# Optimization experiments

Hardware: AMD Instinct MI355X
Metric: run time of the kernel (lower is better)

The kernel has to match this reference:

```python
import jax, jax.numpy as jnp
import numpy as np

THRESHOLD = 0.3
STRENGTH = 0.1
MIN_S = 0.0
MAX_S = 0.5
EPS_COS = 1e-8
EPS_LN = 1e-5

B, T, D = 1024, 64, 256
P = 2048
H = 512


def _layernorm(x, g, b):
    mu = x.mean(-1, keepdims=True)
    var = ((x - mu) ** 2).mean(-1, keepdims=True)
    return (x - mu) * jax.lax.rsqrt(var + EPS_LN) * g + b


def setup_inputs() -> dict:
    key = jax.random.key(0)
    ks = jax.random.split(key, 10)
    s = lambda fan_in: 1.0 / np.sqrt(fan_in)
    return {
        "current_feat": jax.random.normal(ks[0], (B, T, D), jnp.float32),
        "prototype": jax.random.normal(ks[1], (P, T, D), jnp.float32),
        "dd_w1": jax.random.normal(ks[2], (2 * D, H), jnp.float32) * s(2 * D),
        "dd_b1": jnp.zeros((H,), jnp.float32),
        "dd_g1": jnp.ones((H,), jnp.float32),
        "dd_be1": jnp.zeros((H,), jnp.float32),
        "dd_w2": jax.random.normal(ks[3], (H, H // 2), jnp.float32) * s(H),
        "dd_b2": jnp.zeros((H // 2,), jnp.float32),
        "dd_w3": jax.random.normal(ks[4], (H // 2, 1), jnp.float32) * s(H // 2),
        "dd_b3": jnp.zeros((1,), jnp.float32),
        "cal_w1": jax.random.normal(ks[5], (D, H), jnp.float32) * s(D),
        "cal_b1": jnp.zeros((H,), jnp.float32),
        "cal_g1": jnp.ones((H,), jnp.float32),
        "cal_be1": jnp.zeros((H,), jnp.float32),
        "cal_w2": jax.random.normal(ks[6], (H, H), jnp.float32) * s(H),
        "cal_b2": jnp.zeros((H,), jnp.float32),
        "cal_w3": jax.random.normal(ks[7], (H, D), jnp.float32) * s(H),
        "cal_b3": jnp.zeros((D,), jnp.float32),
    }


def reference(current_feat, prototype,
              dd_w1, dd_b1, dd_g1, dd_be1, dd_w2, dd_b2, dd_w3, dd_b3,
              cal_w1, cal_b1, cal_g1, cal_be1, cal_w2, cal_b2, cal_w3, cal_b3):
    # --- drift detection ---
    feat_flat = current_feat.mean(axis=1)          # [B, D]
    proto_centers = prototype.mean(axis=1)         # [P, D]
    fn = jnp.maximum(jnp.linalg.norm(feat_flat, axis=-1), EPS_COS)   # [B]
    pn = jnp.maximum(jnp.linalg.norm(proto_centers, axis=-1), EPS_COS)  # [P]
    sim = jnp.einsum('bd,pd->bp', feat_flat, proto_centers) / (fn[:, None] * pn[None, :])
    drift_score = 1.0 - sim                        # [B, P]
    is_drifted = drift_score.mean(axis=0) > THRESHOLD  # [P] bool

    # --- calibration (batched over all P, then masked scatter) ---
    global_mean = feat_flat.mean(axis=0)           # [D]
    concat = jnp.concatenate(
        [proto_centers, jnp.broadcast_to(global_mean, (proto_centers.shape[0], global_mean.shape[0]))], axis=-1)  # [P, 2D]
    h = jax.nn.relu(_layernorm(concat @ dd_w1 + dd_b1, dd_g1, dd_be1))
    h = jax.nn.relu(h @ dd_w2 + dd_b2)
    drift_conf = jax.nn.sigmoid(h @ dd_w3 + dd_b3)[:, 0]  # [P]

    c = jax.nn.relu(_layernorm(proto_centers @ cal_w1 + cal_b1, cal_g1, cal_be1))
    c = jax.nn.relu(c @ cal_w2 + cal_b2)
    delta = c @ cal_w3 + cal_b3                    # [P, D]

    strength = jnp.clip(STRENGTH * drift_conf, MIN_S, MAX_S)  # [P]
    new_center = proto_centers + strength[:, None] * delta    # [P, D]

    calibrated = jnp.where(is_drifted[:, None, None], new_center[:, None, :], prototype)  # [P, T, D]
    return calibrated, drift_score, is_drifted
```

## Files before the change

kernel.cpp:

```cpp
#include <hip/hip_runtime.h>
#include <hip/hip_bf16.h>
#include <math.h>

#define BB 1024
#define TT 64
#define DD 256
#define PP 2048
#define HH 512

typedef __attribute__((ext_vector_type(8))) short short8;
typedef __attribute__((ext_vector_type(4))) float f32x4;

__device__ __forceinline__ float4 f4add(float4 a, float4 b) {
    return make_float4(a.x + b.x, a.y + b.y, a.z + b.z, a.w + b.w);
}

__device__ __forceinline__ void nt_store4(float* p, float4 v) {
    f32x4 t = {v.x, v.y, v.z, v.w};
    __builtin_nontemporal_store(t, (f32x4*)p);
}

__device__ __forceinline__ void nt_store1(float* p, float v) {
    __builtin_nontemporal_store(v, p);
}

__device__ __forceinline__ float blk_reduce(float v, float* sm) {
    int tid = threadIdx.x;
    #pragma unroll
    for (int o = 32; o > 0; o >>= 1) v += __shfl_down(v, o, 64);
    if ((tid & 63) == 0) sm[tid >> 6] = v;
    __syncthreads();
    float r = sm[0] + sm[1] + sm[2] + sm[3];
    __syncthreads();
    return r;
}

__device__ __forceinline__ float2 blk_reduce2(float a, float b, float* sm) {
    int tid = threadIdx.x;
    #pragma unroll
    for (int o = 32; o > 0; o >>= 1) {
        a += __shfl_down(a, o, 64);
        b += __shfl_down(b, o, 64);
    }
    if ((tid & 63) == 0) { sm[(tid >> 6) * 2] = a; sm[(tid >> 6) * 2 + 1] = b; }
    __syncthreads();
    float ra = sm[0] + sm[2] + sm[4] + sm[6];
    float rb = sm[1] + sm[3] + sm[5] + sm[7];
    __syncthreads();
    return make_float2(ra, rb);
}

__device__ __forceinline__ float row_mean_batch(const float* __restrict__ base,
                                                float* __restrict__ smr) {
    int tid = threadIdx.x;
    int c4 = tid & 63;
    int t0 = tid >> 6;
    const float* p = base + t0 * DD + (c4 << 2);
    float4 v[16];
    #pragma unroll
    for (int i = 0; i < 16; ++i)
        v[i] = *(const float4*)(p + (i << 2) * DD);
    #pragma unroll
    for (int i = 0; i < 8; ++i) v[i] = f4add(v[i], v[i + 8]);
    #pragma unroll
    for (int i = 0; i < 4; ++i) v[i] = f4add(v[i], v[i + 4]);
    float4 s = f4add(f4add(v[0], v[1]), f4add(v[2], v[3]));
    *(float4*)&smr[t0 * 256 + (c4 << 2)] = s;
    __syncthreads();
    return (smr[tid] + smr[256 + tid] + smr[512 + tid] + smr[768 + tid]) * (1.f / TT);
}

__global__ void prep_k(const float* __restrict__ cf, const float* __restrict__ proto,
                       const float* __restrict__ dd_w1, const float* __restrict__ dd_w2,
                       const float* __restrict__ cal_w1, const float* __restrict__ cal_w2,
                       const float* __restrict__ cal_w3,
                       float* __restrict__ ffm, float* __restrict__ fn,
                       float* __restrict__ pn, float* __restrict__ pc,
                       __hip_bfloat16* __restrict__ ffb, __hip_bfloat16* __restrict__ pcb,
                       __hip_bfloat16* __restrict__ w1cat, __hip_bfloat16* __restrict__ w2dd,
                       __hip_bfloat16* __restrict__ w2cal, __hip_bfloat16* __restrict__ w3cal) {
    __shared__ float smr[1024];
    __shared__ float sm[4];
    int b = blockIdx.x, tid = threadIdx.x;
    if (b < 1024) {
        float m = row_mean_batch(cf + (size_t)b * TT * DD, smr);
        ffm[(size_t)b * DD + tid] = m;
        ffb[(size_t)b * DD + tid] = __float2bfloat16(m);
        float q = m * m;
        #pragma unroll
        for (int o = 32; o > 0; o >>= 1) q += __shfl_down(q, o, 64);
        if ((tid & 63) == 0) sm[tid >> 6] = q;
        __syncthreads();
        if (tid == 0) fn[b] = fmaxf(sqrtf(sm[0] + sm[1] + sm[2] + sm[3]), 1e-8f);
    } else if (b < 3072) {
        int r = b - 1024;
        float m = row_mean_batch(proto + (size_t)r * TT * DD, smr);
        pc[(size_t)r * DD + tid] = m;
        pcb[(size_t)r * DD + tid] = __float2bfloat16(m);
        float q = m * m;
        #pragma unroll
        for (int o = 32; o > 0; o >>= 1) q += __shfl_down(q, o, 64);
        if ((tid & 63) == 0) sm[tid >> 6] = q;
        __syncthreads();
        if (tid == 0) pn[r] = fmaxf(sqrtf(sm[0] + sm[1] + sm[2] + sm[3]), 1e-8f);
    } else {
        int idx = (b - 3072) * 256 + tid;
        if (idx < 262144) {
            int half = idx >> 17;
            int i = idx & 131071;
            int n = i & 511, k = i >> 9;
            const float* src = half ? cal_w1 : dd_w1;
            w1cat[(size_t)(half * 512 + n) * 256 + k] = __float2bfloat16(src[(size_t)k * 512 + n]);
        } else if (idx < 393216) {
            int i = idx - 262144;
            int n = i & 255, k = i >> 8;
            w2dd[(size_t)n * 512 + k] = __float2bfloat16(dd_w2[(size_t)k * 256 + n]);
        } else if (idx < 655360) {
            int i = idx - 393216;
            int n = i & 511, k = i >> 9;
            w2cal[(size_t)n * 512 + k] = __float2bfloat16(cal_w2[(size_t)k * 512 + n]);
        } else {
            int i = idx - 655360;
            int n = i & 255, k = i >> 8;
            w3cal[(size_t)n * 512 + k] = __float2bfloat16(cal_w3[(size_t)k * 256 + n]);
        }
    }
}

__global__ void sim_addvec_k(const __hip_bfloat16* __restrict__ A,
                             const __hip_bfloat16* __restrict__ Bt,
                             const float* __restrict__ fn, const float* __restrict__ pn,
                             const float* __restrict__ ffm,
                             const float* __restrict__ dd_w1, const float* __restrict__ dd_b1,
                             float* __restrict__ drift, float* __restrict__ colsum,
                             float* __restrict__ addvec) {
    if (blockIdx.x >= 512) {
        __shared__ float gmk[256];
        int tid = threadIdx.x;
        const float* f = ffm + tid;
        float a0 = 0.f, a1 = 0.f, a2 = 0.f, a3 = 0.f, a4 = 0.f, a5 = 0.f, a6 = 0.f, a7 = 0.f;
        #pragma unroll 4
        for (int b = 0; b < 1024; b += 8) {
            a0 += f[(b + 0) << 8]; a1 += f[(b + 1) << 8];
            a2 += f[(b + 2) << 8]; a3 += f[(b + 3) << 8];
            a4 += f[(b + 4) << 8]; a5 += f[(b + 5) << 8];
            a6 += f[(b + 6) << 8]; a7 += f[(b + 7) << 8];
        }
        gmk[tid] = (((a0 + a1) + (a2 + a3)) + ((a4 + a5) + (a6 + a7))) * (1.f / BB);
        __syncthreads();
        int j = (blockIdx.x - 512) * 256 + tid;
        float s = dd_b1[j];
        #pragma unroll 8
        for (int k = 0; k < 256; ++k) s = fmaf(gmk[k], dd_w1[(size_t)(256 + k) * 512 + j], s);
        addvec[j] = s;
        return;
    }
    int wid = (blockIdx.x << 2) + (threadIdx.x >> 6);
    int lane = threadIdx.x & 63;
    int mw = wid >> 6, nw = wid & 63;
    int m0 = mw << 5, n0 = nw << 5;
    int lr = lane & 15, quad = lane >> 4;
    const __hip_bfloat16* pa0 = A + (size_t)(m0 + lr) * DD + quad * 8;
    const __hip_bfloat16* pa1 = pa0 + 16 * DD;
    const __hip_bfloat16* pb0 = Bt + (size_t)(n0 + lr) * DD + quad * 8;
    const __hip_bfloat16* pb1 = pb0 + 16 * DD;
    f32x4 acc00 = {0,0,0,0}, acc01 = {0,0,0,0}, acc10 = {0,0,0,0}, acc11 = {0,0,0,0};
    #pragma unroll
    for (int k = 0; k < DD; k += 32) {
        short8 a0 = *(const short8*)(pa0 + k);
        short8 a1 = *(const short8*)(pa1 + k);
        short8 b0 = *(const short8*)(pb0 + k);
        short8 b1 = *(const short8*)(pb1 + k);
        acc00 = __builtin_amdgcn_mfma_f32_16x16x32_bf16(a0, b0, acc00, 0, 0, 0);
        acc01 = __builtin_amdgcn_mfma_f32_16x16x32_bf16(a0, b1, acc01, 0, 0, 0);
        acc10 = __builtin_amdgcn_mfma_f32_16x16x32_bf16(a1, b0, acc10, 0, 0, 0);
        acc11 = __builtin_amdgcn_mfma_f32_16x16x32_bf16(a1, b1, acc11, 0, 0, 0);
    }
    int col0 = n0 + lr, col1 = col0 + 16;
    float ip0 = 1.f / pn[col0], ip1 = 1.f / pn[col1];
    float cs0 = 0.f, cs1 = 0.f;
    #pragma unroll
    for (int r = 0; r < 4; ++r) {
        int row0 = m0 + quad * 4 + r;
        int row1 = row0 + 16;
        float if0 = 1.f / fn[row0];
        float if1 = 1.f / fn[row1];
        float d00 = 1.f - acc00[r] * if0 * ip0;
        float d01 = 1.f - acc01[r] * if0 * ip1;
        float d10 = 1.f - acc10[r] * if1 * ip0;
        float d11 = 1.f - acc11[r] * if1 * ip1;
        nt_store1(&drift[(size_t)row0 * PP + col0], d00);
        nt_store1(&drift[(size_t)row0 * PP + col1], d01);
        nt_store1(&drift[(size_t)row1 * PP + col0], d10);
        nt_store1(&drift[(size_t)row1 * PP + col1], d11);
        cs0 += d00 + d10;
        cs1 += d01 + d11;
    }
    cs0 += __shfl_xor(cs0, 16, 64); cs0 += __shfl_xor(cs0, 32, 64);
    cs1 += __shfl_xor(cs1, 16, 64); cs1 += __shfl_xor(cs1, 32, 64);
    if (quad == 0) {
        atomicAdd(&colsum[col0], cs0);
        atomicAdd(&colsum[col1], cs1);
    }
}

template <int K, int OUT_BF16, int RELU>
__device__ __forceinline__ void gemm_tile(const __hip_bfloat16* __restrict__ A,
                                          const __hip_bfloat16* __restrict__ Bt,
                                          const float* __restrict__ bias0,
                                          const float* __restrict__ bias1, int split,
                                          void* __restrict__ Cout, int N, int lognt,
                                          int wid, int lane) {
    int mw = wid >> lognt, nw = wid & ((1 << lognt) - 1);
    int m0 = mw << 5, n0 = nw << 5;
    int lr = lane & 15, quad = lane >> 4;
    const __hip_bfloat16* pa0 = A + (size_t)(m0 + lr) * K + quad * 8;
    const __hip_bfloat16* pa1 = pa0 + 16 * K;
    const __hip_bfloat16* pb0 = Bt + (size_t)(n0 + lr) * K + quad * 8;
    const __hip_bfloat16* pb1 = pb0 + 16 * K;
    f32x4 acc00 = {0,0,0,0}, acc01 = {0,0,0,0}, acc10 = {0,0,0,0}, acc11 = {0,0,0,0};
    #pragma unroll
    for (int k = 0; k < K; k += 32) {
        short8 a0 = *(const short8*)(pa0 + k);
        short8 a1 = *(const short8*)(pa1 + k);
        short8 b0 = *(const short8*)(pb0 + k);
        short8 b1 = *(const short8*)(pb1 + k);
        acc00 = __builtin_amdgcn_mfma_f32_16x16x32_bf16(a0, b0, acc00, 0, 0, 0);
        acc01 = __builtin_amdgcn_mfma_f32_16x16x32_bf16(a0, b1, acc01, 0, 0, 0);
        acc10 = __builtin_amdgcn_mfma_f32_16x16x32_bf16(a1, b0, acc10, 0, 0, 0);
        acc11 = __builtin_amdgcn_mfma_f32_16x16x32_bf16(a1, b1, acc11, 0, 0, 0);
    }
    int col0 = n0 + lr, col1 = col0 + 16;
    float bi0 = (col0 < split) ? bias0[col0] : bias1[col0 - split];
    float bi1 = (col1 < split) ? bias0[col1] : bias1[col1 - split];
    #pragma unroll
    for (int r = 0; r < 4; ++r) {
        int row0 = m0 + quad * 4 + r;
        int row1 = row0 + 16;
        float v00 = acc00[r] + bi0, v01 = acc01[r] + bi1;
        float v10 = acc10[r] + bi0, v11 = acc11[r] + bi1;
        if (RELU) {
            v00 = fmaxf(v00, 0.f); v01 = fmaxf(v01, 0.f);
            v10 = fmaxf(v10, 0.f); v11 = fmaxf(v11, 0.f);
        }
        if (OUT_BF16) {
            __hip_bfloat16* C = (__hip_bfloat16*)Cout;
            C[(size_t)row0 * N + col0] = __float2bfloat16(v00);
            C[(size_t)row0 * N + col1] = __float2bfloat16(v01);
            C[(size_t)row1 * N + col0] = __float2bfloat16(v10);
            C[(size_t)row1 * N + col1] = __float2bfloat16(v11);
        } else {
            float* C = (float*)Cout;
            C[(size_t)row0 * N + col0] = v00;
            C[(size_t)row0 * N + col1] = v01;
            C[(size_t)row1 * N + col0] = v10;
            C[(size_t)row1 * N + col1] = v11;
        }
    }
}

__global__ void gemm1_k(const __hip_bfloat16* __restrict__ pcb,
                        const __hip_bfloat16* __restrict__ w1cat,
                        const float* __restrict__ addvec, const float* __restrict__ cal_b1,
                        float* __restrict__ buf1) {
    int wid = (blockIdx.x << 2) + (threadIdx.x >> 6);
    gemm_tile<256, 0, 0>(pcb, w1cat, addvec, cal_b1, 512, buf1, 1024, 5,
                         wid, threadIdx.x & 63);
}

__global__ void ln2_k(const float* __restrict__ X,
                      __hip_bfloat16* __restrict__ Ydd, __hip_bfloat16* __restrict__ Ycal,
                      const float* __restrict__ gdd, const float* __restrict__ bedd,
                      const float* __restrict__ gcal, const float* __restrict__ becal) {
    __shared__ float sm[8];
    int r = blockIdx.x, tid = threadIdx.x;
    const float* row = X + (size_t)r * 1024;
    {
        float x0 = row[tid], x1 = row[tid + 256];
        float2 t = blk_reduce2(x0 + x1, x0 * x0 + x1 * x1, sm);
        float mu = t.x * (1.f / HH);
        float var = fmaxf(t.y * (1.f / HH) - mu * mu, 0.f);
        float rs = rsqrtf(var + 1e-5f);
        float d0 = x0 - mu, d1 = x1 - mu;
        __hip_bfloat16* y = Ydd + (size_t)r * HH;
        y[tid]       = __float2bfloat16(fmaxf(d0 * rs * gdd[tid] + bedd[tid], 0.f));
        y[tid + 256] = __float2bfloat16(fmaxf(d1 * rs * gdd[tid + 256] + bedd[tid + 256], 0.f));
    }
    {
        float x0 = row[512 + tid], x1 = row[768 + tid];
        float2 t = blk_reduce2(x0 + x1, x0 * x0 + x1 * x1, sm);
        float mu = t.x * (1.f / HH);
        float var = fmaxf(t.y * (1.f / HH) - mu * mu, 0.f);
        float rs = rsqrtf(var + 1e-5f);
        float d0 = x0 - mu, d1 = x1 - mu;
        __hip_bfloat16* y = Ycal + (size_t)r * HH;
        y[tid]       = __float2bfloat16(fmaxf(d0 * rs * gcal[tid] + becal[tid], 0.f));
        y[tid + 256] = __float2bfloat16(fmaxf(d1 * rs * gcal[tid + 256] + becal[tid + 256], 0.f));
    }
}

__global__ void gemm2_k(const __hip_bfloat16* __restrict__ act_dd,
                        const __hip_bfloat16* __restrict__ act_cal,
                        const __hip_bfloat16* __restrict__ w2dd,
                        const __hip_bfloat16* __restrict__ w2cal,
                        const float* __restrict__ dd_b2, const float* __restrict__ cal_b2,
                        __hip_bfloat16* __restrict__ act2b, __hip_bfloat16* __restrict__ act3b) {
    int lane = threadIdx.x & 63;
    if (blockIdx.x < 128) {
        int wid = (blockIdx.x << 2) + (threadIdx.x >> 6);
        gemm_tile<512, 1, 1>(act_dd, w2dd, dd_b2, dd_b2, 1 << 30, act2b, 256, 3, wid, lane);
    } else {
        int wid = ((blockIdx.x - 128) << 2) + (threadIdx.x >> 6);
        gemm_tile<512, 1, 1>(act_cal, w2cal, cal_b2, cal_b2, 1 << 30, act3b, 512, 4, wid, lane);
    }
}

__global__ void gemm3_conf_k(const __hip_bfloat16* __restrict__ act3b,
                             const __hip_bfloat16* __restrict__ w3cal,
                             const float* __restrict__ cal_b3,
                             const __hip_bfloat16* __restrict__ act2b,
                             const float* __restrict__ dd_w3, const float* __restrict__ dd_b3,
                             const float* __restrict__ colsum,
                             float* __restrict__ delta, float* __restrict__ strength,
                             float* __restrict__ out_is) {
    if (blockIdx.x < 128) {
        int wid = (blockIdx.x << 2) + (threadIdx.x >> 6);
        gemm_tile<512, 0, 0>(act3b, w3cal, cal_b3, cal_b3, 1 << 30, delta, 256, 3,
                             wid, threadIdx.x & 63);
        return;
    }
    int p = ((blockIdx.x - 128) << 2) + (threadIdx.x >> 6);
    int lane = threadIdx.x & 63;
    const __hip_bfloat16* row = act2b + (size_t)p * 256 + lane * 4;
    float s = 0.f;
    #pragma unroll
    for (int j = 0; j < 4; ++j)
        s += __bfloat162float(row[j]) * dd_w3[lane * 4 + j];
    #pragma unroll
    for (int o = 32; o > 0; o >>= 1) s += __shfl_down(s, o, 64);
    if (lane == 0) {
        float conf = 1.f / (1.f + expf(-(s + dd_b3[0])));
        strength[p] = fminf(fmaxf(0.1f * conf, 0.f), 0.5f);
        out_is[p] = (colsum[p] * (1.f / BB) > 0.3f) ? 1.f : 0.f;
    }
}

__global__ void finalize_k(const float* __restrict__ pc, const float* __restrict__ delta,
                           const float* __restrict__ strength, const float* __restrict__ colsum,
                           const float* __restrict__ proto, float* __restrict__ out) {
    int p = blockIdx.x;
    int d4 = (threadIdx.x & 63) << 2;
    int t0 = threadIdx.x >> 6;
    bool dr = colsum[p] * (1.f / BB) > 0.3f;
    float* o = out + (size_t)p * TT * DD;
    if (dr) {
        float s = strength[p];
        float4 pcv = *(const float4*)(pc + (size_t)p * DD + d4);
        float4 dv  = *(const float4*)(delta + (size_t)p * DD + d4);
        float4 nc = make_float4(fmaf(s, dv.x, pcv.x), fmaf(s, dv.y, pcv.y),
                                fmaf(s, dv.z, pcv.z), fmaf(s, dv.w, pcv.w));
        #pragma unroll
        for (int t = t0; t < TT; t += 4)
            nt_store4(o + t * DD + d4, nc);
    } else {
        const float* pr = proto + (size_t)p * TT * DD;
        #pragma unroll
        for (int t = t0; t < TT; t += 4)
            nt_store4(o + t * DD + d4, *(const float4*)(pr + t * DD + d4));
    }
}

extern "C" void kernel_launch(void* const* d_in, const int* in_sizes, int n_in,
                              void* d_out, int out_size, void* d_ws, size_t ws_size,
                              hipStream_t stream) {
    const float* cf     = (const float*)d_in[0];
    const float* proto  = (const float*)d_in[1];
    const float* dd_w1  = (const float*)d_in[2];
    const float* dd_b1  = (const float*)d_in[3];
    const float* dd_g1  = (const float*)d_in[4];
    const float* dd_be1 = (const float*)d_in[5];
    const float* dd_w2  = (const float*)d_in[6];
    const float* dd_b2  = (const float*)d_in[7];
    const float* dd_w3  = (const float*)d_in[8];
    const float* dd_b3  = (const float*)d_in[9];
    const float* cal_w1 = (const float*)d_in[10];
    const float* cal_b1 = (const float*)d_in[11];
    const float* cal_g1 = (const float*)d_in[12];
    const float* cal_be1= (const float*)d_in[13];
    const float* cal_w2 = (const float*)d_in[14];
    const float* cal_b2 = (const float*)d_in[15];
    const float* cal_w3 = (const float*)d_in[16];
    const float* cal_b3 = (const float*)d_in[17];

    float* out_cal   = (float*)d_out;
    float* out_drift = out_cal + (size_t)PP * TT * DD;
    float* out_is    = out_drift + (size_t)BB * PP;

    float* w = (float*)d_ws;
    float* colsum   = w;
    float* addvec   = w + 4096;
    float* fn       = w + 4608;
    float* pn       = w + 5632;
    float* strength = w + 7680;
    float* pc       = w + 9728;
    float* buf1     = w + 534016;
    float* ffm      = buf1;
    float* delta    = w + 2631168;
    __hip_bfloat16* bb = (__hip_bfloat16*)(w + 3155456);
    __hip_bfloat16* ffb     = bb;
    __hip_bfloat16* pcb     = bb + 262144;
    __hip_bfloat16* w1cat   = bb + 786432;
    __hip_bfloat16* w2dd    = bb + 1048576;
    __hip_bfloat16* w2cal   = bb + 1179648;
    __hip_bfloat16* w3cal   = bb + 1441792;
    __hip_bfloat16* act_dd  = bb + 1572864;
    __hip_bfloat16* act_cal = bb + 2621440;
    __hip_bfloat16* act2b   = bb + 3670016;
    __hip_bfloat16* act3b   = bb + 4194304;

    hipMemsetAsync(colsum, 0, 2048 * sizeof(float), stream);

    prep_k<<<6144, 256, 0, stream>>>(cf, proto, dd_w1, dd_w2, cal_w1, cal_w2, cal_w3,
                                     ffm, fn, pn, pc, ffb, pcb,
                                     w1cat, w2dd, w2cal, w3cal);
    sim_addvec_k<<<514, 256, 0, stream>>>(ffb, pcb, fn, pn, ffm, dd_w1, dd_b1,
                                          out_drift, colsum, addvec);
    gemm1_k<<<512, 256, 0, stream>>>(pcb, w1cat, addvec, cal_b1, buf1);
    ln2_k<<<PP, 256, 0, stream>>>(buf1, act_dd, act_cal, dd_g1, dd_be1, cal_g1, cal_be1);
    gemm2_k<<<384, 256, 0, stream>>>(act_dd, act_cal, w2dd, w2cal, dd_b2, cal_b2,
                                     act2b, act3b);
    gemm3_conf_k<<<640, 256, 0, stream>>>(act3b, w3cal, cal_b3, act2b, dd_w3, dd_b3,
                                          colsum, delta, strength, out_is);
    finalize_k<<<PP, 256, 0, stream>>>(pc, delta, strength, colsum, proto, out_cal);
}
```

Baseline: 410.2 us.

## Fuse first GEMM with LayerNorm and restructure prep reduction kernel

Merges the first MLP GEMM and the following LayerNorm+ReLU into a single kernel. Each block computes a full 32x512 row tile, and the row statistics are reduced through shuffles and shared memory, so the fp32 intermediate buffer no longer goes through memory. The prep kernel now uses one wave per row for the time-mean, with vector bf16 stores and a barrier-free norm reduction. It also zeroes colsum in place of the separate memset, and each block converts four weight elements. The fused GEMM launches only 128 blocks, which may leave many compute units idle.

```diff
diff --git a/kernel.cpp b/kernel.cpp
--- a/kernel.cpp
+++ b/kernel.cpp
@@ -9,6 +9,7 @@
 #define HH 512
 
 typedef __attribute__((ext_vector_type(8))) short short8;
+typedef __attribute__((ext_vector_type(4))) short short4v;
 typedef __attribute__((ext_vector_type(4))) float f32x4;
 
 __device__ __forceinline__ float4 f4add(float4 a, float4 b) {
@@ -24,50 +25,11 @@
     __builtin_nontemporal_store(v, p);
 }
 
-__device__ __forceinline__ float blk_reduce(float v, float* sm) {
-    int tid = threadIdx.x;
-    #pragma unroll
-    for (int o = 32; o > 0; o >>= 1) v += __shfl_down(v, o, 64);
-    if ((tid & 63) == 0) sm[tid >> 6] = v;
-    __syncthreads();
-    float r = sm[0] + sm[1] + sm[2] + sm[3];
-    __syncthreads();
-    return r;
-}
-
-__device__ __forceinline__ float2 blk_reduce2(float a, float b, float* sm) {
-    int tid = threadIdx.x;
-    #pragma unroll
-    for (int o = 32; o > 0; o >>= 1) {
-        a += __shfl_down(a, o, 64);
-        b += __shfl_down(b, o, 64);
-    }
-    if ((tid & 63) == 0) { sm[(tid >> 6) * 2] = a; sm[(tid >> 6) * 2 + 1] = b; }
-    __syncthreads();
-    float ra = sm[0] + sm[2] + sm[4] + sm[6];
-    float rb = sm[1] + sm[3] + sm[5] + sm[7];
-    __syncthreads();
-    return make_float2(ra, rb);
-}
-
-__device__ __forceinline__ float row_mean_batch(const float* __restrict__ base,
-                                                float* __restrict__ smr) {
-    int tid = threadIdx.x;
-    int c4 = tid & 63;
-    int t0 = tid >> 6;
-    const float* p = base + t0 * DD + (c4 << 2);
-    float4 v[16];
-    #pragma unroll
-    for (int i = 0; i < 16; ++i)
-        v[i] = *(const float4*)(p + (i << 2) * DD);
-    #pragma unroll
-    for (int i = 0; i < 8; ++i) v[i] = f4add(v[i], v[i + 8]);
-    #pragma unroll
-    for (int i = 0; i < 4; ++i) v[i] = f4add(v[i], v[i + 4]);
-    float4 s = f4add(f4add(v[0], v[1]), f4add(v[2], v[3]));
-    *(float4*)&smr[t0 * 256 + (c4 << 2)] = s;
-    __syncthreads();
-    return (smr[tid] + smr[256 + tid] + smr[512 + tid] + smr[768 + tid]) * (1.f / TT);
+__device__ __forceinline__ void store_bf16x4(__hip_bfloat16* dst, float4 m) {
+    union { __hip_bfloat16 h[4]; short4v s; } u;
+    u.h[0] = __float2bfloat16(m.x); u.h[1] = __float2bfloat16(m.y);
+    u.h[2] = __float2bfloat16(m.z); u.h[3] = __float2bfloat16(m.w);
+    *(short4v*)dst = u.s;
 }
 
 __global__ void prep_k(const float* __restrict__ cf, const float* __restrict__ proto,
@@ -76,53 +38,72 @@
                        const float* __restrict__ cal_w3,
                        float* __restrict__ ffm, float* __restrict__ fn,
                        float* __restrict__ pn, float* __restrict__ pc,
+                       float* __restrict__ colsum,
                        __hip_bfloat16* __restrict__ ffb, __hip_bfloat16* __restrict__ pcb,
                        __hip_bfloat16* __restrict__ w1cat, __hip_bfloat16* __restrict__ w2dd,
                        __hip_bfloat16* __restrict__ w2cal, __hip_bfloat16* __restrict__ w3cal) {
-    __shared__ float smr[1024];
-    __shared__ float sm[4];
     int b = blockIdx.x, tid = threadIdx.x;
-    if (b < 1024) {
-        float m = row_mean_batch(cf + (size_t)b * TT * DD, smr);
-        ffm[(size_t)b * DD + tid] = m;
-        ffb[(size_t)b * DD + tid] = __float2bfloat16(m);
-        float q = m * m;
-        #pragma unroll
-        for (int o = 32; o > 0; o >>= 1) q += __shfl_down(q, o, 64);
-        if ((tid & 63) == 0) sm[tid >> 6] = q;
-        __syncthreads();
-        if (tid == 0) fn[b] = fmaxf(sqrtf(sm[0] + sm[1] + sm[2] + sm[3]), 1e-8f);
-    } else if (b < 3072) {
-        int r = b - 1024;
-        float m = row_mean_batch(proto + (size_t)r * TT * DD, smr);
-        pc[(size_t)r * DD + tid] = m;
-        pcb[(size_t)r * DD + tid] = __float2bfloat16(m);
-        float q = m * m;
-        #pragma unroll
-        for (int o = 32; o > 0; o >>= 1) q += __shfl_down(q, o, 64);
-        if ((tid & 63) == 0) sm[tid >> 6] = q;
-        __syncthreads();
-        if (tid == 0) pn[r] = fmaxf(sqrtf(sm[0] + sm[1] + sm[2] + sm[3]), 1e-8f);
+    if (b < 768) {
+        int wv = tid >> 6, lane = tid & 63;
+        int row = (b << 2) + wv;
+        const float* base = (row < 1024) ? cf + (size_t)row * TT * DD
+                                         : proto + (size_t)(row - 1024) * TT * DD;
+        const float* p = base + (lane << 2);
+        float4 acc = make_float4(0.f, 0.f, 0.f, 0.f);
+        float4 v[16];
+        #pragma unroll
+        for (int tb = 0; tb < TT; tb += 16) {
+            #pragma unroll
+            for (int i = 0; i < 16; ++i)
+                v[i] = *(const float4*)(p + (size_t)(tb + i) * DD);
+            #pragma unroll
+            for (int i = 0; i < 8; ++i) v[i] = f4add(v[i], v[i + 8]);
+            #pragma unroll
+            for (int i = 0; i < 4; ++i) v[i] = f4add(v[i], v[i + 4]);
+            acc = f4add(acc, f4add(f4add(v[0], v[1]), f4add(v[2], v[3])));
+        }
+        float4 m = make_float4(acc.x * (1.f / TT), acc.y * (1.f / TT),
+                               acc.z * (1.f / TT), acc.w * (1.f / TT));
+        if (row < 1024) {
+            *(float4*)(ffm + (size_t)row * DD + (lane << 2)) = m;
+            store_bf16x4(ffb + (size_t)row * DD + (lane << 2), m);
+        } else {
+            int r = row - 1024;
+            *(float4*)(pc + (size_t)r * DD + (lane << 2)) = m;
+            store_bf16x4(pcb + (size_t)r * DD + (lane << 2), m);
+        }
+        float q = m.x * m.x + m.y * m.y + m.z * m.z + m.w * m.w;
+        #pragma unroll
+        for (int o = 32; o > 0; o >>= 1) q += __shfl_xor(q, o, 64);
+        if (lane == 0) {
+            float nv = fmaxf(sqrtf(q), 1e-8f);
+            if (row < 1024) fn[row] = nv; else pn[row - 1024] = nv;
+        }
     } else {
-        int idx = (b - 3072) * 256 + tid;
-        if (idx < 262144) {
-            int half = idx >> 17;
-            int i = idx & 131071;
-            int n = i & 511, k = i >> 9;
-            const float* src = half ? cal_w1 : dd_w1;
-            w1cat[(size_t)(half * 512 + n) * 256 + k] = __float2bfloat16(src[(size_t)k * 512 + n]);
-        } else if (idx < 393216) {
-            int i = idx - 262144;
-            int n = i & 255, k = i >> 8;
-            w2dd[(size_t)n * 512 + k] = __float2bfloat16(dd_w2[(size_t)k * 256 + n]);
-        } else if (idx < 655360) {
-            int i = idx - 393216;
-            int n = i & 511, k = i >> 9;
-            w2cal[(size_t)n * 512 + k] = __float2bfloat16(cal_w2[(size_t)k * 512 + n]);
-        } else {
-            int i = idx - 655360;
-            int n = i & 255, k = i >> 8;
-            w3cal[(size_t)n * 512 + k] = __float2bfloat16(cal_w3[(size_t)k * 256 + n]);
+        int bb = b - 768;
+        if (bb < 8) colsum[bb * 256 + tid] = 0.f;
+        #pragma unroll
+        for (int i2 = 0; i2 < 4; ++i2) {
+            int idx = bb * 1024 + i2 * 256 + tid;
+            if (idx < 262144) {
+                int half = idx >> 17;
+                int i = idx & 131071;
+                int n = i & 511, k = i >> 9;
+                const float* src = half ? cal_w1 : dd_w1;
+                w1cat[(size_t)(half * 512 + n) * 256 + k] = __float2bfloat16(src[(size_t)k * 512 + n]);
+            } else if (idx < 393216) {
+                int i = idx - 262144;
+                int n = i & 255, k = i >> 8;
+                w2dd[(size_t)n * 512 + k] = __float2bfloat16(dd_w2[(size_t)k * 256 + n]);
+            } else if (idx < 655360) {
+                int i = idx - 393216;
+                int n = i & 511, k = i >> 9;
+                w2cal[(size_t)n * 512 + k] = __float2bfloat16(cal_w2[(size_t)k * 512 + n]);
+            } else {
+                int i = idx - 655360;
+                int n = i & 255, k = i >> 8;
+                w3cal[(size_t)n * 512 + k] = __float2bfloat16(cal_w3[(size_t)k * 256 + n]);
+            }
         }
     }
 }
@@ -204,6 +185,120 @@
     }
 }
 
+__global__ void gemm1ln_k(const __hip_bfloat16* __restrict__ pcb,
+                          const __hip_bfloat16* __restrict__ w1cat,
+                          const float* __restrict__ addvec, const float* __restrict__ cal_b1,
+                          const float* __restrict__ gdd, const float* __restrict__ bedd,
+                          const float* __restrict__ gcal, const float* __restrict__ becal,
+                          __hip_bfloat16* __restrict__ Ydd, __hip_bfloat16* __restrict__ Ycal) {
+    __shared__ float lds_s[4][32];
+    __shared__ float lds_q[4][32];
+    int h = blockIdx.x >> 6;
+    int r0 = (blockIdx.x & 63) << 5;
+    int wv = threadIdx.x >> 6;
+    int lane = threadIdx.x & 63;
+    int lr = lane & 15, quad = lane >> 4;
+    const float* bias = h ? cal_b1 : addvec;
+    const float* g    = h ? gcal : gdd;
+    const float* be   = h ? becal : bedd;
+    __hip_bfloat16* Y = h ? Ycal : Ydd;
+
+    const __hip_bfloat16* pa0 = pcb + (size_t)(r0 + lr) * DD + quad * 8;
+    const __hip_bfloat16* pa1 = pa0 + 16 * DD;
+
+    f32x4 a00[4], a01[4], a10[4], a11[4];
+    float bi0[4], bi1[4];
+    #pragma unroll
+    for (int t = 0; t < 4; ++t) {
+        int n0g = h * 512 + wv * 128 + t * 32;
+        const __hip_bfloat16* pb0 = w1cat + (size_t)(n0g + lr) * DD + quad * 8;
+        const __hip_bfloat16* pb1 = pb0 + 16 * DD;
+        f32x4 c00 = {0,0,0,0}, c01 = {0,0,0,0}, c10 = {0,0,0,0}, c11 = {0,0,0,0};
+        #pragma unroll
+        for (int k = 0; k < DD; k += 32) {
+            short8 av0 = *(const short8*)(pa0 + k);
+            short8 av1 = *(const short8*)(pa1 + k);
+            short8 bv0 = *(const short8*)(pb0 + k);
+            short8 bv1 = *(const short8*)(pb1 + k);
+            c00 = __builtin_amdgcn_mfma_f32_16x16x32_bf16(av0, bv0, c00, 0, 0, 0);
+            c01 = __builtin_amdgcn_mfma_f32_16x16x32_bf16(av0, bv1, c01, 0, 0, 0);
+            c10 = __builtin_amdgcn_mfma_f32_16x16x32_bf16(av1, bv0, c10, 0, 0, 0);
+            c11 = __builtin_amdgcn_mfma_f32_16x16x32_bf16(av1, bv1, c11, 0, 0, 0);
+        }
+        a00[t] = c00; a01[t] = c01; a10[t] = c10; a11[t] = c11;
+        int cl0 = wv * 128 + t * 32 + lr;
+        bi0[t] = bias[cl0];
+        bi1[t] = bias[cl0 + 16];
+    }
+
+    float ps_lo[4] = {0,0,0,0}, pq_lo[4] = {0,0,0,0};
+    float ps_hi[4] = {0,0,0,0}, pq_hi[4] = {0,0,0,0};
+    #pragma unroll
+    for (int t = 0; t < 4; ++t) {
+        #pragma unroll
+        for (int r = 0; r < 4; ++r) {
+            float v00 = a00[t][r] + bi0[t];
+            float v01 = a01[t][r] + bi1[t];
+            float v10 = a10[t][r] + bi0[t];
+            float v11 = a11[t][r] + bi1[t];
+            a00[t][r] = v00; a01[t][r] = v01; a10[t][r] = v10; a11[t][r] = v11;
+            ps_lo[r] += v00 + v01;  pq_lo[r] += v00 * v00 + v01 * v01;
+            ps_hi[r] += v10 + v11;  pq_hi[r] += v10 * v10 + v11 * v11;
+        }
+    }
+    #pragma unroll
+    for (int mset = 1; mset < 16; mset <<= 1) {
+        #pragma unroll
+        for (int r = 0; r < 4; ++r) {
+            ps_lo[r] += __shfl_xor(ps_lo[r], mset, 64);
+            pq_lo[r] += __shfl_xor(pq_lo[r], mset, 64);
+            ps_hi[r] += __shfl_xor(ps_hi[r], mset, 64);
+            pq_hi[r] += __shfl_xor(pq_hi[r], mset, 64);
+        }
+    }
+    if (lr < 8) {
+        int rr = quad * 4 + (lr & 3) + ((lr >> 2) << 4);
+        lds_s[wv][rr] = (lr >= 4) ? ps_hi[lr & 3] : ps_lo[lr & 3];
+        lds_q[wv][rr] = (lr >= 4) ? pq_hi[lr & 3] : pq_lo[lr & 3];
+    }
+    __syncthreads();
+
+    float mu_lo[4], rs_lo[4], mu_hi[4], rs_hi[4];
+    #pragma unroll
+    for (int r = 0; r < 4; ++r) {
+        int rl = quad * 4 + r;
+        float s = lds_s[0][rl] + lds_s[1][rl] + lds_s[2][rl] + lds_s[3][rl];
+        float q = lds_q[0][rl] + lds_q[1][rl] + lds_q[2][rl] + lds_q[3][rl];
+        float mu = s * (1.f / HH);
+        float var = fmaxf(q * (1.f / HH) - mu * mu, 0.f);
+        mu_lo[r] = mu; rs_lo[r] = rsqrtf(var + 1e-5f);
+        int rh = rl + 16;
+        s = lds_s[0][rh] + lds_s[1][rh] + lds_s[2][rh] + lds_s[3][rh];
+        q = lds_q[0][rh] + lds_q[1][rh] + lds_q[2][rh] + lds_q[3][rh];
+        mu = s * (1.f / HH);
+        var = fmaxf(q * (1.f / HH) - mu * mu, 0.f);
+        mu_hi[r] = mu; rs_hi[r] = rsqrtf(var + 1e-5f);
+    }
+
+    #pragma unroll
+    for (int t = 0; t < 4; ++t) {
+        int c0 = wv * 128 + t * 32 + lr, c1 = c0 + 16;
+        float g0 = g[c0], g1 = g[c1], b0 = be[c0], b1 = be[c1];
+        #pragma unroll
+        for (int r = 0; r < 4; ++r) {
+            int row = r0 + quad * 4 + r;
+            float y00 = fmaxf((a00[t][r] - mu_lo[r]) * rs_lo[r] * g0 + b0, 0.f);
+            float y01 = fmaxf((a01[t][r] - mu_lo[r]) * rs_lo[r] * g1 + b1, 0.f);
+            float y10 = fmaxf((a10[t][r] - mu_hi[r]) * rs_hi[r] * g0 + b0, 0.f);
+            float y11 = fmaxf((a11[t][r] - mu_hi[r]) * rs_hi[r] * g1 + b1, 0.f);
+            Y[(size_t)row * HH + c0]        = __float2bfloat16(y00);
+            Y[(size_t)row * HH + c1]        = __float2bfloat16(y01);
+            Y[(size_t)(row + 16) * HH + c0] = __float2bfloat16(y10);
+            Y[(size_t)(row + 16) * HH + c1] = __float2bfloat16(y11);
+        }
+    }
+}
+
 template <int K, int OUT_BF16, int RELU>
 __device__ __forceinline__ void gemm_tile(const __hip_bfloat16* __restrict__ A,
                                           const __hip_bfloat16* __restrict__ Bt,
@@ -256,46 +351,6 @@
             C[(size_t)row1 * N + col0] = v10;
             C[(size_t)row1 * N + col1] = v11;
         }
-    }
-}
-
-__global__ void gemm1_k(const __hip_bfloat16* __restrict__ pcb,
-                        const __hip_bfloat16* __restrict__ w1cat,
-                        const float* __restrict__ addvec, const float* __restrict__ cal_b1,
-                        float* __restrict__ buf1) {
-    int wid = (blockIdx.x << 2) + (threadIdx.x >> 6);
-    gemm_tile<256, 0, 0>(pcb, w1cat, addvec, cal_b1, 512, buf1, 1024, 5,
-                         wid, threadIdx.x & 63);
-}
-
-__global__ void ln2_k(const float* __restrict__ X,
-                      __hip_bfloat16* __restrict__ Ydd, __hip_bfloat16* __restrict__ Ycal,
-                      const float* __restrict__ gdd, const float* __restrict__ bedd,
-                      const float* __restrict__ gcal, const float* __restrict__ becal) {
-    __shared__ float sm[8];
-    int r = blockIdx.x, tid = threadIdx.x;
-    const float* row = X + (size_t)r * 1024;
-    {
-        float x0 = row[tid], x1 = row[tid + 256];
-        float2 t = blk_reduce2(x0 + x1, x0 * x0 + x1 * x1, sm);
-        float mu = t.x * (1.f / HH);
-        float var = fmaxf(t.y * (1.f / HH) - mu * mu, 0.f);
-        float rs = rsqrtf(var + 1e-5f);
-        float d0 = x0 - mu, d1 = x1 - mu;
-        __hip_bfloat16* y = Ydd + (size_t)r * HH;
-        y[tid]       = __float2bfloat16(fmaxf(d0 * rs * gdd[tid] + bedd[tid], 0.f));
-        y[tid + 256] = __float2bfloat16(fmaxf(d1 * rs * gdd[tid + 256] + bedd[tid + 256], 0.f));
-    }
-    {
-        float x0 = row[512 + tid], x1 = row[768 + tid];
-        float2 t = blk_reduce2(x0 + x1, x0 * x0 + x1 * x1, sm);
-        float mu = t.x * (1.f / HH);
-        float var = fmaxf(t.y * (1.f / HH) - mu * mu, 0.f);
-        float rs = rsqrtf(var + 1e-5f);
-        float d0 = x0 - mu, d1 = x1 - mu;
-        __hip_bfloat16* y = Ycal + (size_t)r * HH;
-        y[tid]       = __float2bfloat16(fmaxf(d0 * rs * gcal[tid] + becal[tid], 0.f));
-        y[tid + 256] = __float2bfloat16(fmaxf(d1 * rs * gcal[tid + 256] + becal[tid + 256], 0.f));
     }
 }
 
@@ -403,8 +458,7 @@
     float* pn       = w + 5632;
     float* strength = w + 7680;
     float* pc       = w + 9728;
-    float* buf1     = w + 534016;
-    float* ffm      = buf1;
+    float* ffm      = w + 534016;
     float* delta    = w + 2631168;
     __hip_bfloat16* bb = (__hip_bfloat16*)(w + 3155456);
     __hip_bfloat16* ffb     = bb;
@@ -418,15 +472,14 @@
     __hip_bfloat16* act2b   = bb + 3670016;
     __hip_bfloat16* act3b   = bb + 4194304;
 
-    hipMemsetAsync(colsum, 0, 2048 * sizeof(float), stream);
-
-    prep_k<<<6144, 256, 0, stream>>>(cf, proto, dd_w1, dd_w2, cal_w1, cal_w2, cal_w3,
-                                     ffm, fn, pn, pc, ffb, pcb,
+    prep_k<<<1536, 256, 0, stream>>>(cf, proto, dd_w1, dd_w2, cal_w1, cal_w2, cal_w3,
+                                     ffm, fn, pn, pc, colsum, ffb, pcb,
                                      w1cat, w2dd, w2cal, w3cal);
     sim_addvec_k<<<514, 256, 0, stream>>>(ffb, pcb, fn, pn, ffm, dd_w1, dd_b1,
                                           out_drift, colsum, addvec);
-    gemm1_k<<<512, 256, 0, stream>>>(pcb, w1cat, addvec, cal_b1, buf1);
-    ln2_k<<<PP, 256, 0, stream>>>(buf1, act_dd, act_cal, dd_g1, dd_be1, cal_g1, cal_be1);
+    gemm1ln_k<<<128, 256, 0, stream>>>(pcb, w1cat, addvec, cal_b1,
+                                       dd_g1, dd_be1, cal_g1, cal_be1,
+                                       act_dd, act_cal);
     gemm2_k<<<384, 256, 0, stream>>>(act_dd, act_cal, w2dd, w2cal, dd_b2, cal_b2,
                                      act2b, act3b);
     gemm3_conf_k<<<640, 256, 0, stream>>>(act3b, w3cal, cal_b3, act2b, dd_w3, dd_b3,
```

Result: slower. 422.5 us (+3.0%).
